# Kernel optimization log

Hardware: AMD Instinct MI355X
Metric: run time of the kernel (lower is better)

## Reference

```python
import jax, jax.numpy as jnp
import numpy as np

ALPHA = 0.2      # leak / integration time constant
E_FRAC = 0.8     # fraction of excitatory units (Dale's law)
NUM_LAYERS = 3


def setup_inputs() -> dict:
    key = jax.random.key(0)
    T, B, IN, H = 128, 64, 512, 1024
    ks = jax.random.split(key, 7)
    inputs = jax.random.normal(ks[0], (T, B, IN), jnp.float32)
    hidden_init = jax.random.uniform(ks[1], (1, B, H), jnp.float32) * 0.1
    # positive weights (clamped-positive in the original EI cell); Dale sign applied in reference
    W_in0 = jax.random.uniform(ks[2], (H, IN), jnp.float32) * (1.0 / np.sqrt(IN))
    W_in1 = jax.random.uniform(ks[3], (H, H), jnp.float32) * (1.0 / np.sqrt(H))
    W_in2 = jax.random.uniform(ks[4], (H, H), jnp.float32) * (1.0 / np.sqrt(H))
    W_rec = jax.random.uniform(ks[5], (NUM_LAYERS, H, H), jnp.float32) * (1.0 / H)
    b = jnp.zeros((NUM_LAYERS, H), jnp.float32)
    return {"inputs": inputs, "hidden_init": hidden_init, "W_in0": W_in0,
            "W_in1": W_in1, "W_in2": W_in2, "W_rec": W_rec, "b": b}


def reference(inputs, hidden_init, W_in0, W_in1, W_in2, W_rec, b):
    H = W_rec.shape[-1]
    ne = int(H * E_FRAC)
    signs = jnp.concatenate([jnp.ones((ne,), inputs.dtype), -jnp.ones((H - ne,), inputs.dtype)])
    e_mask = (signs > 0).astype(inputs.dtype)           # [H], zero out inhibitory feedforward
    # Dale's law: positive magnitudes with fixed presynaptic sign (columns)
    W_eff = jnp.abs(W_rec) * signs[None, None, :]        # [L, H, H]
    W_ins = (jnp.abs(W_in0), jnp.abs(W_in1), jnp.abs(W_in2))
    h0 = hidden_init[0]                                  # [B, H], shared across layers

    def step(carry, x_t):
        hs, vs = carry
        cell_input = x_t
        new_hs, new_vs = [], []
        for j in range(NUM_LAYERS):
            pre = cell_input @ W_ins[j].T + hs[j] @ W_eff[j].T + b[j]
            v = (1.0 - ALPHA) * vs[j] + ALPHA * pre      # leaky preact state
            h = jax.nn.relu(v)
            cell_input = h * e_mask                      # only excitatory units project forward
            new_hs.append(h)
            new_vs.append(v)
        return (tuple(new_hs), tuple(new_vs)), (cell_input, jnp.stack(new_hs))

    init = (tuple(h0 for _ in range(NUM_LAYERS)),
            tuple(jnp.zeros_like(h0) for _ in range(NUM_LAYERS)))
    _, (outputs, hiddens) = jax.lax.scan(step, init, inputs)
    # outputs: [T, B, H]; hiddens: [T, L, B, H] -> per-layer [T+1, B, H] incl. init
    hiddens = jnp.moveaxis(hiddens, 1, 0)                # [L, T, B, H]
    init_stack = jnp.broadcast_to(h0, (NUM_LAYERS, 1) + h0.shape)
    all_hiddens = jnp.concatenate([init_stack, hiddens], axis=1)  # [L, T+1, B, H]
    return outputs, all_hiddens
```

## Files before the change

kernel.cpp:

```cpp
#include <hip/hip_runtime.h>

#define T_STEPS 128
#define BATCH   64
#define INDIM   512
#define HDIM    1024
#define NE      819
#define OUT0_SZ (T_STEPS*BATCH*HDIM)
#define BH      (BATCH*HDIM)
#define ALLH_L  (129*BH)

#define HS_LAY   131072
#define HS_SLOT  393216
#define NSLOT    131
#define XF_T     65536
#define NBLK     192
#define NGRP     8
#define GSZ      24

typedef short bf16x8 __attribute__((ext_vector_type(8)));
typedef short short2v __attribute__((ext_vector_type(2)));
typedef float f32x4  __attribute__((ext_vector_type(4)));
typedef float f32x2  __attribute__((ext_vector_type(2)));

__device__ __forceinline__ short f2bf(float f){
    unsigned u = __float_as_uint(f);
    u += 0x7FFF + ((u >> 16) & 1);
    return (short)(u >> 16);
}
__device__ __forceinline__ float bf2f(short s){
    return __uint_as_float(((unsigned)(unsigned short)s) << 16);
}

__global__ __launch_bounds__(256) void ei_prep_w(const float* __restrict__ Win0,
        const float* __restrict__ Win1, const float* __restrict__ Win2,
        const float* __restrict__ Wrec, short* __restrict__ wf){
    int gid = blockIdx.x * 256 + threadIdx.x;
    int j, local, nkb, kff; const float* Win; short* base;
    if (gid < 196608)      { j=0; local=gid;        nkb=48; kff=512;  Win=Win0; base=wf; }
    else if (gid < 458752) { j=1; local=gid-196608; nkb=64; kff=1024; Win=Win1; base=wf+3145728; }
    else                   { j=2; local=gid-458752; nkb=64; kff=1024; Win=Win2; base=wf+7340032; }
    int lane = local & 63;
    int fi   = local >> 6;
    int kb   = fi % nkb;
    int it   = fi / nkb;
    int i    = it*16 + (lane & 15);
    int k0   = kb*32 + ((lane >> 4) << 3);
    const float* wrec_row = Wrec + ((size_t)j*HDIM + i)*HDIM;
    bf16x8 hv, lv;
    #pragma unroll
    for (int e = 0; e < 8; ++e){
        int k = k0 + e;
        float w;
        if (k < kff){
            w = fabsf(Win[(size_t)i*kff + k]);
            if (j != 0 && k >= NE) w = 0.f;
        } else {
            int kr = k - kff;
            w = fabsf(wrec_row[kr]);
            if (kr >= NE) w = -w;
        }
        short h = f2bf(w);
        hv[e] = h;
        lv[e] = f2bf(w - bf2f(h));
    }
    short* dst = base + (size_t)fi*1024 + lane*8;
    *(bf16x8*)dst         = hv;
    *(bf16x8*)(dst + 512) = lv;
}

__global__ __launch_bounds__(256) void ei_prep_xf(const float* __restrict__ x,
        short* __restrict__ xf){
    int gid = blockIdx.x * 256 + threadIdx.x;
    int lane = gid & 63;
    int bt   = (gid >> 6) & 3;
    int kb   = (gid >> 8) & 15;
    int t    = gid >> 12;
    int b = bt*16 + (lane & 15);
    int k = kb*32 + ((lane >> 4) << 3);
    const float* src = x + ((size_t)t*BATCH + b)*INDIM + k;
    float4 v0 = *(const float4*)src;
    float4 v1 = *(const float4*)(src + 4);
    float f[8] = {v0.x,v0.y,v0.z,v0.w,v1.x,v1.y,v1.z,v1.w};
    bf16x8 hv, lv;
    #pragma unroll
    for (int e = 0; e < 8; ++e){
        short h = f2bf(f[e]);
        hv[e] = h; lv[e] = f2bf(f[e] - bf2f(h));
    }
    short* dst = xf + (size_t)t*XF_T + (((size_t)(kb*4 + bt)) << 9) + lane*8;
    *(bf16x8*)dst            = hv;
    *(bf16x8*)(dst + 32768)  = lv;
}

__global__ __launch_bounds__(256) void ei_init5(const float* __restrict__ h0,
        float* __restrict__ out, short* __restrict__ hf, int* __restrict__ bar){
    int idx = blockIdx.x * 256 + threadIdx.x;
    int l = idx >> 16, r = idx & 0xFFFF;
    out[OUT0_SZ + (size_t)l*ALLH_L + r] = h0[r];
    if (idx < 1024) bar[idx] = 0;
    if (idx < 24576){
        int lane = idx & 63, bt = (idx >> 6) & 3, kb = (idx >> 8) & 31, j = idx >> 13;
        int b = bt*16 + (lane & 15);
        int k = kb*32 + ((lane >> 4) << 3);
        const float* src = h0 + (size_t)b*HDIM + k;
        float4 v0 = *(const float4*)src;
        float4 v1 = *(const float4*)(src + 4);
        float f[8] = {v0.x,v0.y,v0.z,v0.w,v1.x,v1.y,v1.z,v1.w};
        bf16x8 hv, lv;
        #pragma unroll
        for (int e = 0; e < 8; ++e){
            short hh = f2bf(f[e]);
            hv[e] = hh; lv[e] = f2bf(f[e] - bf2f(hh));
        }
        int off = ((kb*4 + bt) << 9) + lane*8;
        short* b0 = hf + (size_t)j*HS_LAY + off;
        *(bf16x8*)b0           = hv;
        *(bf16x8*)(b0 + 65536) = lv;
    }
}

template<int NKW, int NKFF, int FFLO>
__device__ __forceinline__ void step_mm2(
        const short* __restrict__ pff, const short* __restrict__ prec,
        const short* __restrict__ wp0, const short* __restrict__ wp1,
        int kb0, int btbase, int laneo, f32x4 acc[2][2])
{
    bf16x8 wh[2][2], wl[2][2], ah[2][2], al[2][2];
    auto loadW = [&](int kk, int buf){
        const short* a = wp0 + ((kb0 + kk) << 10);
        const short* b = wp1 + ((kb0 + kk) << 10);
        wh[buf][0] = *(const bf16x8*)a; wl[buf][0] = *(const bf16x8*)(a + 512);
        wh[buf][1] = *(const bf16x8*)b; wl[buf][1] = *(const bf16x8*)(b + 512);
    };
    auto loadA = [&](int kk, int buf){
        int kb = kb0 + kk;
        const short* pa; int lo;
        if (kb < NKFF){ pa = pff + (kb << 11); lo = FFLO; }
        else          { pa = prec + ((kb - NKFF) << 11); lo = 65536; }
        ah[buf][0] = *(const bf16x8*)(pa + ((btbase + 0) << 9) + laneo);
        ah[buf][1] = *(const bf16x8*)(pa + ((btbase + 1) << 9) + laneo);
        al[buf][0] = *(const bf16x8*)(pa + lo + ((btbase + 0) << 9) + laneo);
        al[buf][1] = *(const bf16x8*)(pa + lo + ((btbase + 1) << 9) + laneo);
    };
    loadW(0, 0); loadA(0, 0);
    #pragma unroll
    for (int kk = 0; kk < NKW; ++kk){
        if (kk + 1 < NKW){ loadW(kk + 1, (kk + 1) & 1); loadA(kk + 1, (kk + 1) & 1); }
        const int b = kk & 1;
        acc[0][0] = __builtin_amdgcn_mfma_f32_16x16x32_bf16(ah[b][0], wh[b][0], acc[0][0], 0,0,0);
        acc[0][1] = __builtin_amdgcn_mfma_f32_16x16x32_bf16(ah[b][1], wh[b][0], acc[0][1], 0,0,0);
        acc[1][0] = __builtin_amdgcn_mfma_f32_16x16x32_bf16(ah[b][0], wh[b][1], acc[1][0], 0,0,0);
        acc[1][1] = __builtin_amdgcn_mfma_f32_16x16x32_bf16(ah[b][1], wh[b][1], acc[1][1], 0,0,0);
        acc[0][0] = __builtin_amdgcn_mfma_f32_16x16x32_bf16(al[b][0], wh[b][0], acc[0][0], 0,0,0);
        acc[0][1] = __builtin_amdgcn_mfma_f32_16x16x32_bf16(al[b][1], wh[b][0], acc[0][1], 0,0,0);
        acc[1][0] = __builtin_amdgcn_mfma_f32_16x16x32_bf16(al[b][0], wh[b][1], acc[1][0], 0,0,0);
        acc[1][1] = __builtin_amdgcn_mfma_f32_16x16x32_bf16(al[b][1], wh[b][1], acc[1][1], 0,0,0);
        acc[0][0] = __builtin_amdgcn_mfma_f32_16x16x32_bf16(ah[b][0], wl[b][0], acc[0][0], 0,0,0);
        acc[0][1] = __builtin_amdgcn_mfma_f32_16x16x32_bf16(ah[b][1], wl[b][0], acc[0][1], 0,0,0);
        acc[1][0] = __builtin_amdgcn_mfma_f32_16x16x32_bf16(ah[b][0], wl[b][1], acc[1][0], 0,0,0);
        acc[1][1] = __builtin_amdgcn_mfma_f32_16x16x32_bf16(ah[b][1], wl[b][1], acc[1][1], 0,0,0);
    }
}

__global__ __launch_bounds__(512, 2) void ei_persist3(
        const short* __restrict__ xf, const short* __restrict__ wf,
        const float* __restrict__ bias, float* __restrict__ out,
        short* __restrict__ hf, int* __restrict__ bar)
{
    const int bid   = blockIdx.x;
    const int g     = bid & 7;
    const int w     = bid >> 3;
    const int j     = w >> 3;
    const int strip = g*4 + ((w >> 1) & 3);
    const int bhalf = w & 1;
    const int grp   = g;

    const int tx    = threadIdx.x;
    const int wv    = tx >> 6, lane = tx & 63;
    const int laneo = lane * 8;
    const int btbase = bhalf * 2;
    const int it0   = strip * 2;

    const short* wfj = wf + (j == 0 ? 0 : (j == 1 ? 3145728 : 7340032));
    const int nkb  = (j == 0) ? 48 : 64;
    const int NKW  = nkb >> 3;
    const int kb0  = wv * NKW;
    const short* wp0 = wfj + it0*nkb*1024 + laneo;
    const short* wp1 = wp0 + nkb*1024;

    const int bl  = tx >> 4;
    const int il0 = (tx & 15) << 1;
    const int i_g = strip*32 + il0;
    const int b_g = bhalf*32 + bl;
    const f32x2 bb = *(const f32x2*)&bias[j*HDIM + i_g];
    f32x2 vreg = {0.f, 0.f};

    const int kb4 = i_g >> 5, btw = b_g >> 4;
    const int lnw = (b_g & 15) + (((i_g >> 3) & 3) << 4);
    const int hoff = ((kb4*4 + btw) << 9) + lnw*8 + (i_g & 7);

    __shared__ float psum[8][32][34];

    for (int s = 0; s < T_STEPS + 2; ++s){
        const int t = s - j;
        const bool act = (t >= 0) && (t < T_STEPS);
        if (act){
            const short* hfr  = hf + (size_t)s*HS_SLOT;
            const short* prec = (t == 0) ? (hf + (size_t)j*HS_LAY)
                                         : (hfr + (size_t)j*HS_LAY);
            f32x4 acc[2][2] = {{{0.f,0.f,0.f,0.f},{0.f,0.f,0.f,0.f}},
                               {{0.f,0.f,0.f,0.f},{0.f,0.f,0.f,0.f}}};
            if (j == 0)
                step_mm2<6,16,32768>(xf + (size_t)t*XF_T, prec, wp0, wp1, kb0, btbase, laneo, acc);
            else if (j == 1)
                step_mm2<8,32,65536>(hfr, prec, wp0, wp1, kb0, btbase, laneo, acc);
            else
                step_mm2<8,32,65536>(hfr + HS_LAY, prec, wp0, wp1, kb0, btbase, laneo, acc);

            const int r0 = (lane >> 4) << 2, l15 = lane & 15;
            #pragma unroll
            for (int ic = 0; ic < 2; ++ic)
                #pragma unroll
                for (int bt = 0; bt < 2; ++bt)
                    #pragma unroll
                    for (int r = 0; r < 4; ++r)
                        psum[wv][bt*16 + r0 + r][ic*16 + l15] = acc[ic][bt][r];
        }
        __syncthreads();
        if (act){
            float sum0 = 0.f, sum1 = 0.f;
            #pragma unroll
            for (int ww = 0; ww < 8; ++ww){
                f32x2 p = *(f32x2*)&psum[ww][bl][il0];
                sum0 += p[0]; sum1 += p[1];
            }
            vreg[0] = 0.8f*vreg[0] + 0.2f*(sum0 + bb[0]);
            vreg[1] = 0.8f*vreg[1] + 0.2f*(sum1 + bb[1]);
            float h0v = vreg[0] > 0.f ? vreg[0] : 0.f;
            float h1v = vreg[1] > 0.f ? vreg[1] : 0.f;
            f32x2 hv2 = {h0v, h1v};
            *(f32x2*)&out[OUT0_SZ + ((size_t)(j*129 + t + 1))*BH + b_g*HDIM + i_g] = hv2;
            short hh0 = f2bf(h0v), hl0 = f2bf(h0v - bf2f(hh0));
            short hh1 = f2bf(h1v), hl1 = f2bf(h1v - bf2f(hh1));
            int hi2 = (int)(unsigned short)hh0 | ((int)(unsigned short)hh1 << 16);
            int lo2 = (int)(unsigned short)hl0 | ((int)(unsigned short)hl1 << 16);
            short* hww = hf + (size_t)(s + 1)*HS_SLOT + (size_t)j*HS_LAY + hoff;
            asm volatile("global_store_dword %0, %1, off sc0 sc1"
                         :: "v"(hww), "v"(hi2) : "memory");
            asm volatile("global_store_dword %0, %1, off sc0 sc1"
                         :: "v"(hww + 65536), "v"(lo2) : "memory");
            if (j == 2){
                f32x2 o2 = {(i_g < NE) ? h0v : 0.f, (i_g + 1 < NE) ? h1v : 0.f};
                *(f32x2*)&out[(size_t)t*BH + b_g*HDIM + i_g] = o2;
            }
        }
        if (s == T_STEPS + 1) break;
        asm volatile("s_waitcnt vmcnt(0)" ::: "memory");
        __syncthreads();
        if (tx == 0){
            int prev = __hip_atomic_fetch_add(&bar[grp*32], 1,
                        __ATOMIC_RELAXED, __HIP_MEMORY_SCOPE_AGENT);
            if (prev == (s + 1)*GSZ - 1){
                int sp = __hip_atomic_fetch_add(&bar[256], 1,
                        __ATOMIC_RELAXED, __HIP_MEMORY_SCOPE_AGENT);
                if (sp == (s + 1)*NGRP - 1){
                    #pragma unroll
                    for (int gg = 0; gg < NGRP; ++gg)
                        __hip_atomic_store(&bar[512 + gg*32], s + 1,
                                __ATOMIC_RELAXED, __HIP_MEMORY_SCOPE_AGENT);
                }
            }
            while (__hip_atomic_load(&bar[512 + grp*32],
                    __ATOMIC_RELAXED, __HIP_MEMORY_SCOPE_AGENT) < s + 1)
                __builtin_amdgcn_s_sleep(2);
        }
        __syncthreads();
    }
}

#define HS_PAR_FB 393216
__global__ __launch_bounds__(256) void ei_init3(const float* __restrict__ h0,
        float* __restrict__ out, float* __restrict__ v_ws, short* __restrict__ hfb){
    int idx = blockIdx.x * 256 + threadIdx.x;
    int l = idx >> 16, r = idx & 0xFFFF;
    float h = h0[r];
    out[OUT0_SZ + (size_t)l*ALLH_L + r] = h;
    v_ws[idx] = 0.f;
    if (idx < 24576){
        int lane = idx & 63, bt = (idx >> 6) & 3, kb = (idx >> 8) & 31, j = idx >> 13;
        int b = bt*16 + (lane & 15);
        int k = kb*32 + ((lane >> 4) << 3);
        const float* src = h0 + (size_t)b*HDIM + k;
        float4 v0 = *(const float4*)src;
        float4 v1 = *(const float4*)(src + 4);
        float f[8] = {v0.x,v0.y,v0.z,v0.w,v1.x,v1.y,v1.z,v1.w};
        bf16x8 hv, lv;
        #pragma unroll
        for (int e = 0; e < 8; ++e){
            short hh = f2bf(f[e]);
            hv[e] = hh; lv[e] = f2bf(f[e] - bf2f(hh));
        }
        int off = ((kb*4 + bt) << 9) + lane*8;
        short* b0 = hfb + (size_t)j*HS_LAY + off;
        *(bf16x8*)b0           = hv;
        *(bf16x8*)(b0 + 65536) = lv;
        short* b1 = b0 + HS_PAR_FB;
        *(bf16x8*)b1           = hv;
        *(bf16x8*)(b1 + 65536) = lv;
    }
}

template<int NKW, int NKFF, int FFLO>
__device__ __forceinline__ void stage_body5(
        const short* __restrict__ pff, const short* __restrict__ prec,
        const short* __restrict__ wp, int kb0, int laneo, f32x4 acc[4])
{
    bf16x8 wbh[NKW], wbl[NKW];
    #pragma unroll
    for (int kk = 0; kk < NKW; ++kk){
        const short* w0 = wp + ((kb0 + kk) << 10);
        wbh[kk] = *(const bf16x8*)w0;
        wbl[kk] = *(const bf16x8*)(w0 + 512);
    }
    bf16x8 ah[2][4], al[2][4];
    auto loadA = [&](int kk, int buf){
        int kb = kb0 + kk;
        const short* pa; int lo;
        if (kb < NKFF){ pa = pff + (kb << 11); lo = FFLO; }
        else          { pa = prec + ((kb - NKFF) << 11); lo = 65536; }
        #pragma unroll
        for (int bt = 0; bt < 4; ++bt){
            ah[buf][bt] = *(const bf16x8*)(pa + (bt << 9) + laneo);
            al[buf][bt] = *(const bf16x8*)(pa + lo + (bt << 9) + laneo);
        }
    };
    loadA(0, 0);
    #pragma unroll
    for (int kk = 0; kk < NKW; ++kk){
        if (kk + 1 < NKW) loadA(kk + 1, (kk + 1) & 1);
        const int bf = kk & 1;
        #pragma unroll
        for (int bt = 0; bt < 4; ++bt)
            acc[bt] = __builtin_amdgcn_mfma_f32_16x16x32_bf16(ah[bf][bt], wbh[kk], acc[bt], 0,0,0);
        #pragma unroll
        for (int bt = 0; bt < 4; ++bt)
            acc[bt] = __builtin_amdgcn_mfma_f32_16x16x32_bf16(al[bf][bt], wbh[kk], acc[bt], 0,0,0);
        #pragma unroll
        for (int bt = 0; bt < 4; ++bt)
            acc[bt] = __builtin_amdgcn_mfma_f32_16x16x32_bf16(ah[bf][bt], wbl[kk], acc[bt], 0,0,0);
    }
}

__global__ __launch_bounds__(512, 2) void ei_stage5(
        const short* __restrict__ xf, const short* __restrict__ wf,
        const float* __restrict__ bias, float* __restrict__ out,
        float* __restrict__ v_ws, short* __restrict__ hfb, int s)
{
    int j = blockIdx.x >> 6;
    int t = s - j;
    if (t < 0 || t >= T_STEPS) return;
    int it = blockIdx.x & 63;
    int wv = threadIdx.x >> 6, lane = threadIdx.x & 63;
    int laneo = lane * 8;
    int par_r = (s - 1) & 1, par_w = s & 1;
    const short* hfr  = hfb + par_r*HS_PAR_FB;
    const short* prec = hfr + j*HS_LAY;

    f32x4 acc[4] = {{0.f,0.f,0.f,0.f},{0.f,0.f,0.f,0.f},
                    {0.f,0.f,0.f,0.f},{0.f,0.f,0.f,0.f}};

    if (j == 0){
        const short* pff = xf + t*XF_T;
        const short* wp  = wf + it*48*1024 + laneo;
        stage_body5<6,16,32768>(pff, prec, wp, wv*6, laneo, acc);
    } else if (j == 1){
        const short* pff = hfr;
        const short* wp  = wf + 3145728 + it*64*1024 + laneo;
        stage_body5<8,32,65536>(pff, prec, wp, wv*8, laneo, acc);
    } else {
        const short* pff = hfr + HS_LAY;
        const short* wp  = wf + 7340032 + it*64*1024 + laneo;
        stage_body5<8,32,65536>(pff, prec, wp, wv*8, laneo, acc);
    }

    __shared__ float psum[8][64][18];
    {
        int r0 = (lane >> 4) << 2, l15 = lane & 15;
        #pragma unroll
        for (int bt = 0; bt < 4; ++bt)
            #pragma unroll
            for (int r = 0; r < 4; ++r)
                psum[wv][bt*16 + r0 + r][l15] = acc[bt][r];
    }
    __syncthreads();

    int tx  = threadIdx.x;
    int b   = tx >> 3;
    int il0 = (tx & 7) << 1;
    float* allh = out + OUT0_SZ + ((size_t)(j*129 + t + 1))*BH;
    float* outp = out + (size_t)t*BH;
    short* hww  = hfb + par_w*HS_PAR_FB + j*HS_LAY;
    float sum0 = 0.f, sum1 = 0.f;
    #pragma unroll
    for (int w = 0; w < 8; ++w){
        f32x2 p = *(f32x2*)&psum[w][b][il0];
        sum0 += p[0]; sum1 += p[1];
    }
    int i = it*16 + il0;
    f32x2 bb = *(const f32x2*)&bias[j*HDIM + i];
    int vo = (j*BATCH + b)*HDIM + i;
    f32x2 vold = *(f32x2*)&v_ws[vo];
    float vn0 = 0.8f * vold[0] + 0.2f * (sum0 + bb[0]);
    float vn1 = 0.8f * vold[1] + 0.2f * (sum1 + bb[1]);
    f32x2 vnv = {vn0, vn1};
    *(f32x2*)&v_ws[vo] = vnv;
    float h0 = vn0 > 0.f ? vn0 : 0.f;
    float h1 = vn1 > 0.f ? vn1 : 0.f;
    f32x2 hv2 = {h0, h1};
    *(f32x2*)&allh[b*HDIM + i] = hv2;
    short hh0 = f2bf(h0), hl0 = f2bf(h0 - bf2f(hh0));
    short hh1 = f2bf(h1), hl1 = f2bf(h1 - bf2f(hh1));
    int kb  = i >> 5, btw = b >> 4;
    int lnw = (b & 15) + (((i >> 3) & 3) << 4);
    int off = ((kb*4 + btw) << 9) + lnw*8 + (i & 7);
    short2v hi2 = {hh0, hh1}, lo2 = {hl0, hl1};
    *(short2v*)(hww + off)         = hi2;
    *(short2v*)(hww + off + 65536) = lo2;
    if (j == 2){
        f32x2 o2 = {(i < NE) ? h0 : 0.f, (i + 1 < NE) ? h1 : 0.f};
        *(f32x2*)&outp[b*HDIM + i] = o2;
    }
}

extern "C" void kernel_launch(void* const* d_in, const int* in_sizes, int n_in,
                              void* d_out, int out_size, void* d_ws, size_t ws_size,
                              hipStream_t stream) {
    const float* xin  = (const float*)d_in[0];
    const float* h0   = (const float*)d_in[1];
    const float* Win0 = (const float*)d_in[2];
    const float* Win1 = (const float*)d_in[3];
    const float* Win2 = (const float*)d_in[4];
    const float* Wrec = (const float*)d_in[5];
    const float* bias = (const float*)d_in[6];
    float* out  = (float*)d_out;
    char* ws    = (char*)d_ws;

    const size_t HF_B   = (size_t)NSLOT * HS_SLOT * 2ULL;
    const size_t need_p = 4096 + HF_B + 16777216ULL + 23068672ULL;
    const size_t need_f = 786432ULL + 1572864ULL + 16777216ULL + 23068672ULL;

    if (ws_size >= need_p) {
        int*   bar = (int*)ws;
        short* hf  = (short*)(ws + 4096);
        short* xf  = (short*)(ws + 4096 + HF_B);
        short* wfp = (short*)(ws + 4096 + HF_B + 16777216ULL);
        hipLaunchKernelGGL(ei_prep_w, dim3(2816), dim3(256), 0, stream,
                           Win0, Win1, Win2, Wrec, wfp);
        hipLaunchKernelGGL(ei_prep_xf, dim3(2048), dim3(256), 0, stream, xin, xf);
        hipLaunchKernelGGL(ei_init5, dim3(768), dim3(256), 0, stream, h0, out, hf, bar);
        hipLaunchKernelGGL(ei_persist3, dim3(NBLK), dim3(512), 0, stream,
                           xf, wfp, bias, out, hf, bar);
    } else {
        float* v_ws = (float*)ws;
        short* hfb  = (short*)(ws + 786432);
        short* xf   = (short*)(ws + 786432 + 1572864ULL);
        short* wfp  = (short*)(ws + 786432 + 1572864ULL + 16777216ULL);
        hipLaunchKernelGGL(ei_prep_w, dim3(2816), dim3(256), 0, stream,
                           Win0, Win1, Win2, Wrec, wfp);
        hipLaunchKernelGGL(ei_prep_xf, dim3(2048), dim3(256), 0, stream, xin, xf);
        hipLaunchKernelGGL(ei_init3, dim3(768), dim3(256), 0, stream, h0, out, v_ws, hfb);
        for (int s = 0; s < T_STEPS + 2; ++s)
            hipLaunchKernelGGL(ei_stage5, dim3(192), dim3(512), 0, stream,
                               xf, wfp, bias, out, v_ws, hfb, s);
    }
}
```

Baseline: 1.079 ms.

## Replace global grid barrier with per-layer per-step dataflow flags

The persistent kernel used to hit a hierarchical grid-wide barrier after every wavefront step, so all 192 blocks waited on each other. It now keeps one counter per (layer, step). Each block waits only for the 64 blocks of the previous layer at the previous step and the 64 blocks of its own layer at the previous step, then increments its own flag. This drops the idle skew steps and lets layers run ahead. The barrier workspace grows to 64KB and is zeroed in init, and correctness now depends on memory ordering under relaxed atomics plus the earlier vmcnt wait.

```diff
diff --git a/kernel.cpp b/kernel.cpp
--- a/kernel.cpp
+++ b/kernel.cpp
@@ -14,8 +14,6 @@
 #define NSLOT    131
 #define XF_T     65536
 #define NBLK     192
-#define NGRP     8
-#define GSZ      24
 
 typedef short bf16x8 __attribute__((ext_vector_type(8)));
 typedef short short2v __attribute__((ext_vector_type(2)));
@@ -97,7 +95,7 @@
     int idx = blockIdx.x * 256 + threadIdx.x;
     int l = idx >> 16, r = idx & 0xFFFF;
     out[OUT0_SZ + (size_t)l*ALLH_L + r] = h0[r];
-    if (idx < 1024) bar[idx] = 0;
+    if (idx < 16384) bar[idx] = 0;
     if (idx < 24576){
         int lane = idx & 63, bt = (idx >> 6) & 3, kb = (idx >> 8) & 31, j = idx >> 13;
         int b = bt*16 + (lane & 15);
@@ -162,7 +160,7 @@
     }
 }
 
-__global__ __launch_bounds__(512, 2) void ei_persist3(
+__global__ __launch_bounds__(512, 2) void ei_persist4(
         const short* __restrict__ xf, const short* __restrict__ wf,
         const float* __restrict__ bias, float* __restrict__ out,
         short* __restrict__ hf, int* __restrict__ bar)
@@ -173,7 +171,6 @@
     const int j     = w >> 3;
     const int strip = g*4 + ((w >> 1) & 3);
     const int bhalf = w & 1;
-    const int grp   = g;
 
     const int tx    = threadIdx.x;
     const int wv    = tx >> 6, lane = tx & 63;
@@ -201,22 +198,37 @@
 
     __shared__ float psum[8][32][34];
 
-    for (int s = 0; s < T_STEPS + 2; ++s){
+    for (int s = j; s < j + T_STEPS; ++s){
         const int t = s - j;
-        const bool act = (t >= 0) && (t < T_STEPS);
-        if (act){
-            const short* hfr  = hf + (size_t)s*HS_SLOT;
-            const short* prec = (t == 0) ? (hf + (size_t)j*HS_LAY)
-                                         : (hfr + (size_t)j*HS_LAY);
-            f32x4 acc[2][2] = {{{0.f,0.f,0.f,0.f},{0.f,0.f,0.f,0.f}},
-                               {{0.f,0.f,0.f,0.f},{0.f,0.f,0.f,0.f}}};
-            if (j == 0)
-                step_mm2<6,16,32768>(xf + (size_t)t*XF_T, prec, wp0, wp1, kb0, btbase, laneo, acc);
-            else if (j == 1)
-                step_mm2<8,32,65536>(hfr, prec, wp0, wp1, kb0, btbase, laneo, acc);
-            else
-                step_mm2<8,32,65536>(hfr + HS_LAY, prec, wp0, wp1, kb0, btbase, laneo, acc);
-
+        if (tx == 0){
+            if (j > 0){
+                const int f = ((j - 1)*130 + (s - 1))*32;
+                while (__hip_atomic_load(&bar[f], __ATOMIC_RELAXED,
+                        __HIP_MEMORY_SCOPE_AGENT) < 64)
+                    __builtin_amdgcn_s_sleep(1);
+            }
+            if (t > 0){
+                const int f = (j*130 + (s - 1))*32;
+                while (__hip_atomic_load(&bar[f], __ATOMIC_RELAXED,
+                        __HIP_MEMORY_SCOPE_AGENT) < 64)
+                    __builtin_amdgcn_s_sleep(1);
+            }
+        }
+        __syncthreads();
+
+        const short* hfr  = hf + (size_t)s*HS_SLOT;
+        const short* prec = (t == 0) ? (hf + (size_t)j*HS_LAY)
+                                     : (hfr + (size_t)j*HS_LAY);
+        f32x4 acc[2][2] = {{{0.f,0.f,0.f,0.f},{0.f,0.f,0.f,0.f}},
+                           {{0.f,0.f,0.f,0.f},{0.f,0.f,0.f,0.f}}};
+        if (j == 0)
+            step_mm2<6,16,32768>(xf + (size_t)t*XF_T, prec, wp0, wp1, kb0, btbase, laneo, acc);
+        else if (j == 1)
+            step_mm2<8,32,65536>(hfr, prec, wp0, wp1, kb0, btbase, laneo, acc);
+        else
+            step_mm2<8,32,65536>(hfr + HS_LAY, prec, wp0, wp1, kb0, btbase, laneo, acc);
+
+        {
             const int r0 = (lane >> 4) << 2, l15 = lane & 15;
             #pragma unroll
             for (int ic = 0; ic < 2; ++ic)
@@ -227,7 +239,7 @@
                         psum[wv][bt*16 + r0 + r][ic*16 + l15] = acc[ic][bt][r];
         }
         __syncthreads();
-        if (act){
+        {
             float sum0 = 0.f, sum1 = 0.f;
             #pragma unroll
             for (int ww = 0; ww < 8; ++ww){
@@ -254,27 +266,12 @@
                 *(f32x2*)&out[(size_t)t*BH + b_g*HDIM + i_g] = o2;
             }
         }
-        if (s == T_STEPS + 1) break;
         asm volatile("s_waitcnt vmcnt(0)" ::: "memory");
         __syncthreads();
         if (tx == 0){
-            int prev = __hip_atomic_fetch_add(&bar[grp*32], 1,
-                        __ATOMIC_RELAXED, __HIP_MEMORY_SCOPE_AGENT);
-            if (prev == (s + 1)*GSZ - 1){
-                int sp = __hip_atomic_fetch_add(&bar[256], 1,
-                        __ATOMIC_RELAXED, __HIP_MEMORY_SCOPE_AGENT);
-                if (sp == (s + 1)*NGRP - 1){
-                    #pragma unroll
-                    for (int gg = 0; gg < NGRP; ++gg)
-                        __hip_atomic_store(&bar[512 + gg*32], s + 1,
-                                __ATOMIC_RELAXED, __HIP_MEMORY_SCOPE_AGENT);
-                }
-            }
-            while (__hip_atomic_load(&bar[512 + grp*32],
-                    __ATOMIC_RELAXED, __HIP_MEMORY_SCOPE_AGENT) < s + 1)
-                __builtin_amdgcn_s_sleep(2);
-        }
-        __syncthreads();
+            __hip_atomic_fetch_add(&bar[(j*130 + s)*32], 1,
+                    __ATOMIC_RELAXED, __HIP_MEMORY_SCOPE_AGENT);
+        }
     }
 }
 
@@ -446,19 +443,18 @@
     char* ws    = (char*)d_ws;
 
     const size_t HF_B   = (size_t)NSLOT * HS_SLOT * 2ULL;
-    const size_t need_p = 4096 + HF_B + 16777216ULL + 23068672ULL;
-    const size_t need_f = 786432ULL + 1572864ULL + 16777216ULL + 23068672ULL;
+    const size_t need_p = 65536 + HF_B + 16777216ULL + 23068672ULL;
 
     if (ws_size >= need_p) {
         int*   bar = (int*)ws;
-        short* hf  = (short*)(ws + 4096);
-        short* xf  = (short*)(ws + 4096 + HF_B);
-        short* wfp = (short*)(ws + 4096 + HF_B + 16777216ULL);
+        short* hf  = (short*)(ws + 65536);
+        short* xf  = (short*)(ws + 65536 + HF_B);
+        short* wfp = (short*)(ws + 65536 + HF_B + 16777216ULL);
         hipLaunchKernelGGL(ei_prep_w, dim3(2816), dim3(256), 0, stream,
                            Win0, Win1, Win2, Wrec, wfp);
         hipLaunchKernelGGL(ei_prep_xf, dim3(2048), dim3(256), 0, stream, xin, xf);
         hipLaunchKernelGGL(ei_init5, dim3(768), dim3(256), 0, stream, h0, out, hf, bar);
-        hipLaunchKernelGGL(ei_persist3, dim3(NBLK), dim3(512), 0, stream,
+        hipLaunchKernelGGL(ei_persist4, dim3(NBLK), dim3(512), 0, stream,
                            xf, wfp, bias, out, hf, bar);
     } else {
         float* v_ws = (float*)ws;
```

Measured after the change: 1.195 ms. 10.7% more time.
